# Optimization experiments

Hardware: AMD Instinct MI355X
Metric: run time of the kernel (lower is better)

The kernel has to match this reference:

```python
import jax, jax.numpy as jnp
import numpy as np

N = 50000       # num vertices
E_SEG = 80000   # num hyperedges
NNZ = 400000    # incidence pairs
FIN = 512       # input feature dim
H = 256         # MLP_hidden
C = 40          # num classes
NLAYER = 2      # All_num_layers
ALPHA = 0.5     # restart_alpha


def _w(k, shape):
    return jax.random.normal(k, shape, jnp.float32) * (1.0 / np.sqrt(shape[0]))


def setup_inputs() -> dict:
    key = jax.random.key(0)
    ks = jax.random.split(key, 12)
    return {
        "x": jax.random.normal(ks[0], (N, FIN), jnp.float32),
        "vertex": jax.random.randint(ks[1], (NNZ,), 0, N),
        "edges": jax.random.randint(ks[2], (NNZ,), 0, E_SEG),
        "lin_in_w": _w(ks[3], (FIN, H)), "lin_in_b": jnp.zeros((H,), jnp.float32),
        "w1": _w(ks[4], (H, H)),   "b1": jnp.zeros((H,), jnp.float32),
        "w2": _w(ks[5], (2 * H, H)), "b2": jnp.zeros((H,), jnp.float32),
        "w3": _w(ks[6], (H, H)),   "b3": jnp.zeros((H,), jnp.float32),
        "cls_w1": _w(ks[7], (H, H)), "cls_b1": jnp.zeros((H,), jnp.float32),
        "cls_w2": _w(ks[8], (H, C)), "cls_b2": jnp.zeros((C,), jnp.float32),
    }


def reference(x, vertex, edges, lin_in_w, lin_in_b, w1, b1, w2, b2, w3, b3,
              cls_w1, cls_b1, cls_w2, cls_b2):
    # input projection (dropout is identity at p=0)
    x = jax.nn.relu(x @ lin_in_w + lin_in_b)           # [N, H]
    x0 = x
    for _ in range(NLAYER):  # same conv weights reused each layer
        # W1 (1-layer MLP = Linear), gather to incidences
        xve = (x @ w1 + b1)[vertex]                    # [NNZ, H]
        # scatter-add to hyperedges
        xe = jax.ops.segment_sum(xve, edges, num_segments=E_SEG)  # [E, H]
        # gather back, concat with vertex feats, W2 (Linear on 2H)
        xev = jnp.concatenate([x[vertex], xe[edges]], axis=-1) @ w2 + b2  # [NNZ, H]
        # scatter-add to vertices
        xv = jax.ops.segment_sum(xev, vertex, num_segments=N)     # [N, H]
        # restart connection + W (Linear) + outer activation
        x = (1.0 - ALPHA) * xv + ALPHA * x0
        x = jax.nn.relu(x @ w3 + b3)
    # classifier MLP (2 layers: Linear -> relu -> Linear)
    h = jax.nn.relu(x @ cls_w1 + cls_b1)
    return h @ cls_w2 + cls_b2                          # [N, C]
```

## Files before the change

kernel.cpp:

```cpp
#include <hip/hip_runtime.h>
#include <hip/hip_bf16.h>
#include <cstdint>
#include <cstddef>

#define HD   256
#define NV   50000
#define NE   80000
#define NNZC 400000
#define FINC 512
#define NCLS 40

using bf16 = __hip_bfloat16;

typedef short bf16x8v __attribute__((ext_vector_type(8)));
typedef float f32x4   __attribute__((ext_vector_type(4)));

#define NCH_E ((NE + 1023) / 1024)
#define NCH_V ((NV + 1023) / 1024)

__device__ __forceinline__ float b2f(unsigned short u) {
    union { unsigned int i; float f; } c; c.i = ((unsigned int)u) << 16; return c.f;
}
__device__ __forceinline__ unsigned short f2b(float f) {
    union { float f; unsigned int i; } c; c.f = f;
    return (unsigned short)((c.i + 0x7FFFu + ((c.i >> 16) & 1u)) >> 16);
}
__device__ __forceinline__ float4 load4f(const bf16* p) {
    ushort4 u = *reinterpret_cast<const ushort4*>(p);
    return make_float4(b2f(u.x), b2f(u.y), b2f(u.z), b2f(u.w));
}
__device__ __forceinline__ void store4(bf16* p, float4 v) {
    ushort4 u; u.x = f2b(v.x); u.y = f2b(v.y); u.z = f2b(v.z); u.w = f2b(v.w);
    *reinterpret_cast<ushort4*>(p) = u;
}

__device__ __forceinline__ void gl_lds16(const bf16* g, short* l) {
    __builtin_amdgcn_global_load_lds(
        (const __attribute__((address_space(1))) unsigned int*)g,
        (__attribute__((address_space(3))) unsigned int*)l,
        16, 0, 0);
}

__global__ __launch_bounds__(256)
void fill0_k(unsigned int* __restrict__ p, long long n)
{
    long long i = (long long)blockIdx.x * 256 + threadIdx.x;
    long long stride = (long long)gridDim.x * 256;
    for (; i < n; i += stride) p[i] = 0u;
}

__global__ __launch_bounds__(256)
void hist_k(const int* __restrict__ vertex, const int* __restrict__ edges,
            int* __restrict__ cnt_v, int* __restrict__ cnt_e, int nnz)
{
    int i = blockIdx.x * 256 + threadIdx.x;
    if (i < nnz) {
        atomicAdd(&cnt_v[vertex[i]], 1);
        atomicAdd(&cnt_e[edges[i]], 1);
    }
}

__global__ __launch_bounds__(256)
void scan_part2_k(const int* __restrict__ cnt_e, int* __restrict__ off_e, int* __restrict__ part_e,
                  const int* __restrict__ cnt_v, int* __restrict__ off_v, int* __restrict__ part_v)
{
    const int* cnt; int* off; int* part; int n;
    if (blockIdx.y == 0) { cnt = cnt_e; off = off_e; part = part_e; n = NE; }
    else                 { cnt = cnt_v; off = off_v; part = part_v; n = NV; }
    int base = blockIdx.x * 1024;
    if (base >= n) return;
    __shared__ int s[256];
    int idx = base + threadIdx.x * 4;
    int v[4], sum = 0;
    #pragma unroll
    for (int j = 0; j < 4; ++j) { v[j] = (idx + j < n) ? cnt[idx + j] : 0; sum += v[j]; }
    s[threadIdx.x] = sum;
    __syncthreads();
    #pragma unroll
    for (int d = 1; d < 256; d <<= 1) {
        int t = (threadIdx.x >= d) ? s[threadIdx.x - d] : 0;
        __syncthreads();
        s[threadIdx.x] += t;
        __syncthreads();
    }
    int excl = s[threadIdx.x] - sum;
    #pragma unroll
    for (int j = 0; j < 4; ++j) {
        if (idx + j < n) off[idx + j] = excl;
        excl += v[j];
    }
    if (threadIdx.x == 255) part[blockIdx.x] = s[255];
}

__global__ __launch_bounds__(256)
void scan_top2_k(int* __restrict__ part_e, int* __restrict__ end_e,
                 int* __restrict__ part_v, int* __restrict__ end_v)
{
    int* part; int* endp; int nch;
    if (blockIdx.x == 0) { part = part_e; endp = end_e; nch = NCH_E; }
    else                 { part = part_v; endp = end_v; nch = NCH_V; }
    __shared__ int s[256];
    int v = (threadIdx.x < nch) ? part[threadIdx.x] : 0;
    s[threadIdx.x] = v;
    __syncthreads();
    #pragma unroll
    for (int d = 1; d < 256; d <<= 1) {
        int t = (threadIdx.x >= d) ? s[threadIdx.x - d] : 0;
        __syncthreads();
        s[threadIdx.x] += t;
        __syncthreads();
    }
    if (threadIdx.x < nch) part[threadIdx.x] = s[threadIdx.x] - v;
    if (threadIdx.x == 255) *endp = s[255];
}

__global__ __launch_bounds__(256)
void scan_addcur2_k(int* __restrict__ off_e, const int* __restrict__ part_e, int* __restrict__ cur_e,
                    int* __restrict__ off_v, const int* __restrict__ part_v, int* __restrict__ cur_v)
{
    int n; int* off; const int* part; int* cur;
    if (blockIdx.y == 0) { n = NE; off = off_e; part = part_e; cur = cur_e; }
    else                 { n = NV; off = off_v; part = part_v; cur = cur_v; }
    int i = blockIdx.x * 256 + threadIdx.x;
    if (i < n) { int o = off[i] + part[i >> 10]; off[i] = o; cur[i] = o; }
}

__global__ __launch_bounds__(256)
void csr_fill_k(const int* __restrict__ vertex, const int* __restrict__ edges,
                int* __restrict__ cur_e, int* __restrict__ cur_v,
                int* __restrict__ adj_e, int* __restrict__ adj_v, int nnz)
{
    int i = blockIdx.x * 256 + threadIdx.x;
    if (i >= nnz) return;
    int v = vertex[i], e = edges[i];
    adj_e[atomicAdd(&cur_e[e], 1)] = v;
    adj_v[atomicAdd(&cur_v[v], 1)] = e;
}

__global__ __launch_bounds__(256)
void dege2_k(const int* __restrict__ cnt_e, const int* __restrict__ adj_v,
             const int* __restrict__ off_v, int* __restrict__ dege2, int n)
{
    int v = blockIdx.x * 256 + threadIdx.x;
    if (v >= n) return;
    int s = 0;
    for (int j = off_v[v]; j < off_v[v + 1]; ++j) s += cnt_e[adj_v[j]];
    dege2[v] = s;
}

__global__ __launch_bounds__(256)
void b1w23_k(const float* __restrict__ b1, const unsigned short* __restrict__ W23bt,
             float* __restrict__ o)
{
    int n = threadIdx.x;
    float s = 0.f;
    for (int k = 0; k < 256; ++k) s += b1[k] * b2f(W23bt[n * 256 + k]);
    o[n] = s;
}

__global__ __launch_bounds__(256)
void prep_w_k(const float* __restrict__ lin_w, const float* __restrict__ w1,
              const float* __restrict__ w2, const float* __restrict__ w3,
              const float* __restrict__ cw1, const float* __restrict__ cw2,
              const float* __restrict__ b2,
              unsigned short* __restrict__ lin_wt, unsigned short* __restrict__ w1_nb,
              unsigned short* __restrict__ w2a_nb, unsigned short* __restrict__ w2b_nb,
              unsigned short* __restrict__ w3t, unsigned short* __restrict__ cw1t,
              unsigned short* __restrict__ cw2t, float* __restrict__ b2w3)
{
    int idx = blockIdx.x * 256 + threadIdx.x;
    if (idx < 131072) { int n = idx >> 9, k = idx & 511; lin_wt[idx] = f2b(lin_w[k * 256 + n]); return; }
    idx -= 131072;
    if (idx < 65536) { w1_nb[idx] = f2b(w1[idx]); return; }
    idx -= 65536;
    if (idx < 65536) { w2a_nb[idx] = f2b(w2[idx]); return; }
    idx -= 65536;
    if (idx < 65536) { w2b_nb[idx] = f2b(w2[65536 + idx]); return; }
    idx -= 65536;
    if (idx < 65536) { int n = idx >> 8, k = idx & 255; w3t[idx] = f2b(w3[k * 256 + n]); return; }
    idx -= 65536;
    if (idx < 65536) { int n = idx >> 8, k = idx & 255; cw1t[idx] = f2b(cw1[k * 256 + n]); return; }
    idx -= 65536;
    if (idx < 12288) { int n = idx >> 8, k = idx & 255; cw2t[idx] = f2b((n < NCLS) ? cw2[k * NCLS + n] : 0.f); return; }
    idx -= 12288;
    if (idx < 256) {
        float s = 0.f;
        for (int k = 0; k < 256; ++k) s += b2[k] * w3[k * 256 + idx];
        b2w3[idx] = s;
    }
}

template<int EPI, bool AF32>
__global__ __launch_bounds__(256)
void mgemm_k(const void* __restrict__ Agv, const bf16* __restrict__ Bt,
             const float* __restrict__ bias, const float* __restrict__ bias2,
             const int* __restrict__ deg, const int* __restrict__ dege2,
             const bf16* __restrict__ Sb, const bf16* __restrict__ z0b,
             const float* __restrict__ b2w3v, const float* __restrict__ b1w23v,
             bf16* __restrict__ Cg, bf16* __restrict__ Cg2, bf16* __restrict__ Cg3,
             int M, int K, int Nc)
{
    const int nbn = Nc >> 7;
    const int nbm = (M + 127) >> 7;
    const int p   = blockIdx.x;
    const int xcd = p & 7;
    const int q   = p >> 3;
    const int cblk = q % nbn;
    const int rblk = q / nbn;
    const int rb   = rblk * 8 + xcd;
    if (rb >= nbm) return;
    const int bn = cblk * 128;
    const int bm = rb * 128;

    __shared__ __align__(16) short As[128 * 64];
    __shared__ __align__(16) short Bs[128 * 64];

    const int t  = threadIdx.x;
    const int wv = t >> 6, l = t & 63;
    const int wr = wv >> 1, wc = wv & 1;
    const int l15 = l & 15;

    f32x4 acc[4][4];
    #pragma unroll
    for (int m = 0; m < 4; ++m)
        #pragma unroll
        for (int n = 0; n < 4; ++n)
            acc[m][n] = (f32x4){0.f, 0.f, 0.f, 0.f};

    const int brow8   = l >> 3;
    const int bcol_sw = (((l & 7) ^ (l >> 3)) * 8);

    for (int k0 = 0; k0 < K; k0 += 64) {
        if constexpr (AF32) {
            const float* Af = (const float*)Agv;
            #pragma unroll
            for (int pi = 0; pi < 4; ++pi) {
                int idx8 = pi * 256 + t;
                int row  = idx8 >> 3;
                int cg   = (idx8 & 7) * 8;
                int ga = bm + row; if (ga >= M) ga = M - 1;
                const float* src = Af + (size_t)ga * K + k0 + cg;
                f32x4 u = *reinterpret_cast<const f32x4*>(src);
                f32x4 v = *reinterpret_cast<const f32x4*>(src + 4);
                bf16x8v o;
                o[0] = (short)f2b(u[0]); o[1] = (short)f2b(u[1]);
                o[2] = (short)f2b(u[2]); o[3] = (short)f2b(u[3]);
                o[4] = (short)f2b(v[0]); o[5] = (short)f2b(v[1]);
                o[6] = (short)f2b(v[2]); o[7] = (short)f2b(v[3]);
                *reinterpret_cast<bf16x8v*>(As + row * 64 + (cg ^ ((row & 7) * 8))) = o;
            }
        } else {
            const bf16* Ab = (const bf16*)Agv;
            #pragma unroll
            for (int i = 0; i < 4; ++i) {
                int c = wv * 4 + i;
                int row = c * 8 + brow8;
                int ga = bm + row; if (ga >= M) ga = M - 1;
                gl_lds16(Ab + (size_t)ga * K + k0 + bcol_sw, As + c * 512);
            }
        }
        #pragma unroll
        for (int i = 0; i < 4; ++i) {
            int c = wv * 4 + i;
            int row = c * 8 + brow8;
            gl_lds16(Bt + (size_t)(bn + row) * K + k0 + bcol_sw, Bs + c * 512);
        }
        __syncthreads();

        #pragma unroll
        for (int ks = 0; ks < 2; ++ks) {
            bf16x8v a[4], b[4];
            const int kb = ks * 64 + (l >> 4) * 16;
            #pragma unroll
            for (int m = 0; m < 4; ++m) {
                int r = wr * 64 + m * 16 + l15;
                a[m] = *reinterpret_cast<const bf16x8v*>(
                           (const char*)As + r * 128 + (kb ^ ((r & 7) << 4)));
            }
            #pragma unroll
            for (int n = 0; n < 4; ++n) {
                int r = wc * 64 + n * 16 + l15;
                b[n] = *reinterpret_cast<const bf16x8v*>(
                           (const char*)Bs + r * 128 + (kb ^ ((r & 7) << 4)));
            }
            #pragma unroll
            for (int m = 0; m < 4; ++m)
                #pragma unroll
                for (int n = 0; n < 4; ++n)
                    acc[m][n] = __builtin_amdgcn_mfma_f32_16x16x32_bf16(a[m], b[n], acc[m][n], 0, 0, 0);
        }
        __syncthreads();
    }

    if (EPI == 3) {
        int oi = bn >> 8;
        bf16* CC = (oi == 0) ? Cg : (oi == 1) ? Cg2 : Cg3;
        const float* bb = (oi == 0) ? bias : (oi == 1) ? bias2 : nullptr;
        int cb = bn & 255;
        float bv[4];
        #pragma unroll
        for (int n = 0; n < 4; ++n)
            bv[n] = bb ? bb[cb + wc * 64 + n * 16 + l15] : 0.f;
        #pragma unroll
        for (int m = 0; m < 4; ++m) {
            #pragma unroll
            for (int i = 0; i < 4; ++i) {
                int row = bm + wr * 64 + m * 16 + (l >> 4) * 4 + i;
                if (row >= M) continue;
                size_t base = (size_t)row * 256 + cb + wc * 64 + l15;
                #pragma unroll
                for (int n = 0; n < 4; ++n)
                    reinterpret_cast<unsigned short*>(CC)[base + n * 16] = f2b(acc[m][n][i] + bv[n]);
            }
        }
    } else if (EPI == 4) {
        float bv[4], bw[4], bb1[4];
        #pragma unroll
        for (int n = 0; n < 4; ++n) {
            int col = bn + wc * 64 + n * 16 + l15;
            bv[n]  = bias[col];
            bw[n]  = b2w3v[col];
            bb1[n] = b1w23v[col];
        }
        #pragma unroll
        for (int m = 0; m < 4; ++m) {
            #pragma unroll
            for (int i = 0; i < 4; ++i) {
                int row = bm + wr * 64 + m * 16 + (l >> 4) * 4 + i;
                if (row >= M) continue;
                float d   = (float)deg[row];
                float de2 = (float)dege2[row];
                size_t base = (size_t)row * Nc + bn + wc * 64 + l15;
                #pragma unroll
                for (int n = 0; n < 4; ++n) {
                    size_t idx = base + (size_t)n * 16;
                    float sv = b2f(reinterpret_cast<const unsigned short*>(Sb)[idx]);
                    float zv = b2f(reinterpret_cast<const unsigned short*>(z0b)[idx]);
                    float v = 0.5f * (d * (sv + bw[n]) + acc[m][n][i] + de2 * bb1[n])
                              + 0.5f * zv + bv[n];
                    v = fmaxf(v, 0.f);
                    reinterpret_cast<unsigned short*>(Cg)[idx] = f2b(v);
                }
            }
        }
    } else {
        float bv[4];
        #pragma unroll
        for (int n = 0; n < 4; ++n)
            bv[n] = bias ? bias[bn + wc * 64 + n * 16 + l15] : 0.f;
        #pragma unroll
        for (int m = 0; m < 4; ++m) {
            #pragma unroll
            for (int i = 0; i < 4; ++i) {
                int row = bm + wr * 64 + m * 16 + (l >> 4) * 4 + i;
                if (row >= M) continue;
                size_t base = (size_t)row * Nc + bn + wc * 64 + l15;
                #pragma unroll
                for (int n = 0; n < 4; ++n) {
                    float v = acc[m][n][i] + bv[n];
                    if (EPI == 1) v = fmaxf(v, 0.f);
                    reinterpret_cast<unsigned short*>(Cg)[base + n * 16] = f2b(v);
                }
            }
        }
    }
}

__global__ __launch_bounds__(256)
void gather_sum_k(const bf16* __restrict__ src, const int* __restrict__ adj,
                  const int* __restrict__ off, bf16* __restrict__ dst, int nseg)
{
    int seg = blockIdx.x * 4 + (threadIdx.x >> 6);
    if (seg >= nseg) return;
    int lane = threadIdx.x & 63;
    int s0 = off[seg], s1 = off[seg + 1];
    float4 acc = make_float4(0.f, 0.f, 0.f, 0.f);
    int j = s0;
    for (; j + 4 <= s1; j += 4) {
        int r0 = adj[j], r1 = adj[j + 1], r2 = adj[j + 2], r3 = adj[j + 3];
        float4 v0 = load4f(src + (size_t)r0 * HD + lane * 4);
        float4 v1 = load4f(src + (size_t)r1 * HD + lane * 4);
        float4 v2 = load4f(src + (size_t)r2 * HD + lane * 4);
        float4 v3 = load4f(src + (size_t)r3 * HD + lane * 4);
        acc.x += (v0.x + v1.x) + (v2.x + v3.x);
        acc.y += (v0.y + v1.y) + (v2.y + v3.y);
        acc.z += (v0.z + v1.z) + (v2.z + v3.z);
        acc.w += (v0.w + v1.w) + (v2.w + v3.w);
    }
    for (; j < s1; ++j) {
        float4 v = load4f(src + (size_t)adj[j] * HD + lane * 4);
        acc.x += v.x; acc.y += v.y; acc.z += v.z; acc.w += v.w;
    }
    store4(dst + (size_t)seg * HD + lane * 4, acc);
}

__global__ __launch_bounds__(256)
void cls_mfma_k(const bf16* __restrict__ Hm, const bf16* __restrict__ Wt,
                const float* __restrict__ bias, float* __restrict__ out, int M)
{
    const int wv = threadIdx.x >> 6, l = threadIdx.x & 63;
    const int l15 = l & 15;
    const int r0 = blockIdx.x * 64 + wv * 16;
    f32x4 acc[3];
    #pragma unroll
    for (int n = 0; n < 3; ++n) acc[n] = (f32x4){0.f, 0.f, 0.f, 0.f};

    int arow = r0 + l15; if (arow >= M) arow = M - 1;
    const int ko = (l >> 4) * 8;
    for (int kk = 0; kk < HD; kk += 32) {
        bf16x8v a = *reinterpret_cast<const bf16x8v*>(Hm + (size_t)arow * HD + kk + ko);
        #pragma unroll
        for (int n = 0; n < 3; ++n) {
            bf16x8v b = *reinterpret_cast<const bf16x8v*>(Wt + (size_t)(n * 16 + l15) * HD + kk + ko);
            acc[n] = __builtin_amdgcn_mfma_f32_16x16x32_bf16(a, b, acc[n], 0, 0, 0);
        }
    }
    #pragma unroll
    for (int n = 0; n < 3; ++n) {
        int col = n * 16 + l15;
        if (col >= NCLS) continue;
        float bv = bias[col];
        #pragma unroll
        for (int i = 0; i < 4; ++i) {
            int row = r0 + (l >> 4) * 4 + i;
            if (row < M) out[(size_t)row * NCLS + col] = acc[n][i] + bv;
        }
    }
}

static inline int xcd_grid(int M, int Nc)
{
    int nbm = (M + 127) >> 7;
    int nbn = Nc >> 7;
    return nbn * (((nbm + 7) / 8) * 8);
}

extern "C" void kernel_launch(void* const* d_in, const int* in_sizes, int n_in,
                              void* d_out, int out_size, void* d_ws, size_t ws_size,
                              hipStream_t stream)
{
    const float* x_in   = (const float*)d_in[0];
    const int*   vertex = (const int*)d_in[1];
    const int*   edges  = (const int*)d_in[2];
    const float* lin_w  = (const float*)d_in[3];
    const float* lin_b  = (const float*)d_in[4];
    const float* w1     = (const float*)d_in[5];
    const float* b1     = (const float*)d_in[6];
    const float* w2     = (const float*)d_in[7];
    const float* b2     = (const float*)d_in[8];
    const float* w3     = (const float*)d_in[9];
    const float* b3     = (const float*)d_in[10];
    const float* cw1    = (const float*)d_in[11];
    const float* cb1    = (const float*)d_in[12];
    const float* cw2    = (const float*)d_in[13];
    const float* cb2    = (const float*)d_in[14];
    float* out = (float*)d_out;
    (void)in_sizes; (void)n_in; (void)out_size; (void)ws_size;

    char* ws = (char*)d_ws;
    const size_t nvhd = (size_t)NV * HD, nehd = (size_t)NE * HD;
    size_t off = 0;
    auto alloc = [&](size_t bytes) { char* p = ws + off; off += (bytes + 255) & ~(size_t)255; return p; };
    bf16* x0 = (bf16*)alloc(nvhd * 2);
    bf16* xA = (bf16*)alloc(nvhd * 2);
    bf16* E1 = (bf16*)alloc(nehd * 2);
    bf16* E2 = (bf16*)alloc(nehd * 2);
    bf16* S  = (bf16*)alloc(nvhd * 2);
    bf16* z0 = (bf16*)alloc(nvhd * 2);
    unsigned short* W23at  = (unsigned short*)alloc(2 * 256 * 256 * 2);
    unsigned short* w3t    = W23at + 65536;
    unsigned short* W23bt  = (unsigned short*)alloc(256 * 256 * 2);
    unsigned short* W123bt = (unsigned short*)alloc(256 * 256 * 2);
    unsigned short* w2ab   = (unsigned short*)alloc(512 * 256 * 2);
    unsigned short* w2a_nb = w2ab;
    unsigned short* w2b_nb = w2ab + 256 * 256;
    unsigned short* w1_nb  = (unsigned short*)alloc(256 * 256 * 2);
    unsigned short* lin_wt = (unsigned short*)alloc(256 * 512 * 2);
    unsigned short* cw1t   = (unsigned short*)alloc(256 * 256 * 2);
    unsigned short* cw2t   = (unsigned short*)alloc(48 * 256 * 2);
    float* b2w3  = (float*)alloc(256 * 4);
    float* b1w23 = (float*)alloc(256 * 4);
    int* cnt_e = (int*)alloc(NE * 4);
    int* cnt_v = (int*)alloc(NV * 4);
    int* dege2 = (int*)alloc(NV * 4);
    int* off_e = (int*)alloc((NE + 1) * 4);
    int* off_v = (int*)alloc((NV + 1) * 4);
    int* cur_e = (int*)alloc(NE * 4);
    int* cur_v = (int*)alloc(NV * 4);
    int* part_e = (int*)alloc(256 * 4);
    int* part_v = (int*)alloc(256 * 4);
    int* adj_e = (int*)alloc((size_t)NNZC * 4);
    int* adj_v = (int*)alloc((size_t)NNZC * 4);

    dim3 blk(256);

    fill0_k<<<128, blk, 0, stream>>>((unsigned int*)cnt_e, NE + NV);
    hist_k<<<(NNZC + 255) / 256, blk, 0, stream>>>(vertex, edges, cnt_v, cnt_e, NNZC);
    scan_part2_k<<<dim3(NCH_E, 2), blk, 0, stream>>>(cnt_e, off_e, part_e, cnt_v, off_v, part_v);
    scan_top2_k<<<2, blk, 0, stream>>>(part_e, off_e + NE, part_v, off_v + NV);
    scan_addcur2_k<<<dim3((NE + 255) / 256, 2), blk, 0, stream>>>(off_e, part_e, cur_e,
                                                                  off_v, part_v, cur_v);
    csr_fill_k<<<(NNZC + 255) / 256, blk, 0, stream>>>(vertex, edges, cur_e, cur_v, adj_e, adj_v, NNZC);
    dege2_k<<<(NV + 255) / 256, blk, 0, stream>>>(cnt_e, adj_v, off_v, dege2, NV);

    prep_w_k<<<1841, blk, 0, stream>>>(lin_w, w1, w2, w3, cw1, cw2, b2,
                                       lin_wt, w1_nb, w2a_nb, w2b_nb, w3t, cw1t, cw2t, b2w3);
    mgemm_k<3, false><<<xcd_grid(256, 512), blk, 0, stream>>>((const bf16*)w3t, (const bf16*)w2ab,
        nullptr, nullptr, nullptr, nullptr, nullptr, nullptr, nullptr, nullptr,
        (bf16*)W23at, (bf16*)W23bt, nullptr, 256, 256, 512);
    mgemm_k<0, false><<<xcd_grid(256, 256), blk, 0, stream>>>((const bf16*)W23bt, (const bf16*)w1_nb,
        nullptr, nullptr, nullptr, nullptr, nullptr, nullptr, nullptr, nullptr,
        (bf16*)W123bt, nullptr, nullptr, 256, 256, 256);
    b1w23_k<<<1, blk, 0, stream>>>(b1, W23bt, b1w23);

    mgemm_k<1, true><<<xcd_grid(NV, 256), blk, 0, stream>>>(x_in, (const bf16*)lin_wt,
        lin_b, nullptr, nullptr, nullptr, nullptr, nullptr, nullptr, nullptr,
        x0, nullptr, nullptr, NV, FINC, HD);

    const bf16* cur = x0;
    for (int layer = 0; layer < 2; ++layer) {
        if (layer == 0) {
            mgemm_k<3, false><<<xcd_grid(NV, 512), blk, 0, stream>>>(cur, (const bf16*)W23at,
                nullptr, nullptr, nullptr, nullptr, nullptr, nullptr, nullptr, nullptr,
                S, z0, nullptr, NV, HD, 512);
        } else {
            mgemm_k<0, false><<<xcd_grid(NV, 256), blk, 0, stream>>>(cur, (const bf16*)W23at,
                nullptr, nullptr, nullptr, nullptr, nullptr, nullptr, nullptr, nullptr,
                S, nullptr, nullptr, NV, HD, HD);
        }
        gather_sum_k<<<(NE + 3) / 4, blk, 0, stream>>>(cur, adj_e, off_e, E2, NE);
        gather_sum_k<<<(NV + 3) / 4, blk, 0, stream>>>(E2, adj_v, off_v, E1, NV);
        mgemm_k<4, false><<<xcd_grid(NV, 256), blk, 0, stream>>>(E1, (const bf16*)W123bt,
            b3, nullptr, cnt_v, dege2, S, z0, b2w3, b1w23,
            xA, nullptr, nullptr, NV, HD, HD);
        cur = xA;
    }

    mgemm_k<1, false><<<xcd_grid(NV, 256), blk, 0, stream>>>(xA, (const bf16*)cw1t,
        cb1, nullptr, nullptr, nullptr, nullptr, nullptr, nullptr, nullptr,
        E1, nullptr, nullptr, NV, HD, HD);
    cls_mfma_k<<<(NV + 63) / 64, blk, 0, stream>>>(E1, (const bf16*)cw2t, cb2, out, NV);
}
```

Measured before the change: 474.5 us.

## Store S and z0 intermediates in fragment-permuted layout for vectorized epilogue access

```diff
diff --git a/kernel.cpp b/kernel.cpp
--- a/kernel.cpp
+++ b/kernel.cpp
@@ -14,9 +14,11 @@
 
 typedef short bf16x8v __attribute__((ext_vector_type(8)));
 typedef float f32x4   __attribute__((ext_vector_type(4)));
+typedef unsigned short u16x8 __attribute__((ext_vector_type(8)));
 
 #define NCH_E ((NE + 1023) / 1024)
 #define NCH_V ((NV + 1023) / 1024)
+#define NBM_V ((NV + 127) / 128)
 
 __device__ __forceinline__ float b2f(unsigned short u) {
     union { unsigned int i; float f; } c; c.i = ((unsigned int)u) << 16; return c.f;
@@ -292,26 +294,23 @@
         __syncthreads();
     }
 
-    if (EPI == 3) {
+    if (EPI == 5) {
         int oi = bn >> 8;
-        bf16* CC = (oi == 0) ? Cg : (oi == 1) ? Cg2 : Cg3;
-        const float* bb = (oi == 0) ? bias : (oi == 1) ? bias2 : nullptr;
-        int cb = bn & 255;
-        float bv[4];
-        #pragma unroll
-        for (int n = 0; n < 4; ++n)
-            bv[n] = bb ? bb[cb + wc * 64 + n * 16 + l15] : 0.f;
+        bf16* CC = (oi == 0) ? Cg : Cg2;
+        int c2 = (bn >> 7) & 1;
+        unsigned short* P = (unsigned short*)CC + ((size_t)(rb * 2 + c2) * 256 + t) * 64;
         #pragma unroll
         for (int m = 0; m < 4; ++m) {
-            #pragma unroll
-            for (int i = 0; i < 4; ++i) {
-                int row = bm + wr * 64 + m * 16 + (l >> 4) * 4 + i;
-                if (row >= M) continue;
-                size_t base = (size_t)row * 256 + cb + wc * 64 + l15;
+            u16x8 o0, o1;
+            #pragma unroll
+            for (int n = 0; n < 2; ++n)
                 #pragma unroll
-                for (int n = 0; n < 4; ++n)
-                    reinterpret_cast<unsigned short*>(CC)[base + n * 16] = f2b(acc[m][n][i] + bv[n]);
-            }
+                for (int i = 0; i < 4; ++i) {
+                    o0[n * 4 + i] = f2b(acc[m][n][i]);
+                    o1[n * 4 + i] = f2b(acc[m][n + 2][i]);
+                }
+            *reinterpret_cast<u16x8*>(P + m * 16)     = o0;
+            *reinterpret_cast<u16x8*>(P + m * 16 + 8) = o1;
         }
     } else if (EPI == 4) {
         float bv[4], bw[4], bb1[4];
@@ -321,6 +320,14 @@
             bv[n]  = bias[col];
             bw[n]  = b2w3v[col];
             bb1[n] = b1w23v[col];
+        }
+        const unsigned short* Sp = (const unsigned short*)Sb + ((size_t)(rb * 2 + cblk) * 256 + t) * 64;
+        const unsigned short* Zp = (const unsigned short*)z0b + ((size_t)(rb * 2 + cblk) * 256 + t) * 64;
+        u16x8 sv8[8], zv8[8];
+        #pragma unroll
+        for (int j = 0; j < 8; ++j) {
+            sv8[j] = *reinterpret_cast<const u16x8*>(Sp + j * 8);
+            zv8[j] = *reinterpret_cast<const u16x8*>(Zp + j * 8);
         }
         #pragma unroll
         for (int m = 0; m < 4; ++m) {
@@ -333,14 +340,35 @@
                 size_t base = (size_t)row * Nc + bn + wc * 64 + l15;
                 #pragma unroll
                 for (int n = 0; n < 4; ++n) {
-                    size_t idx = base + (size_t)n * 16;
-                    float sv = b2f(reinterpret_cast<const unsigned short*>(Sb)[idx]);
-                    float zv = b2f(reinterpret_cast<const unsigned short*>(z0b)[idx]);
+                    int e = m * 16 + n * 4 + i;
+                    float sv = b2f(sv8[e >> 3][e & 7]);
+                    float zv = b2f(zv8[e >> 3][e & 7]);
                     float v = 0.5f * (d * (sv + bw[n]) + acc[m][n][i] + de2 * bb1[n])
                               + 0.5f * zv + bv[n];
                     v = fmaxf(v, 0.f);
-                    reinterpret_cast<unsigned short*>(Cg)[idx] = f2b(v);
+                    reinterpret_cast<unsigned short*>(Cg)[base + (size_t)n * 16] = f2b(v);
                 }
+            }
+        }
+    } else if (EPI == 3) {
+        int oi = bn >> 8;
+        bf16* CC = (oi == 0) ? Cg : (oi == 1) ? Cg2 : Cg3;
+        const float* bb = (oi == 0) ? bias : (oi == 1) ? bias2 : nullptr;
+        int cb = bn & 255;
+        float bv[4];
+        #pragma unroll
+        for (int n = 0; n < 4; ++n)
+            bv[n] = bb ? bb[cb + wc * 64 + n * 16 + l15] : 0.f;
+        #pragma unroll
+        for (int m = 0; m < 4; ++m) {
+            #pragma unroll
+            for (int i = 0; i < 4; ++i) {
+                int row = bm + wr * 64 + m * 16 + (l >> 4) * 4 + i;
+                if (row >= M) continue;
+                size_t base = (size_t)row * 256 + cb + wc * 64 + l15;
+                #pragma unroll
+                for (int n = 0; n < 4; ++n)
+                    reinterpret_cast<unsigned short*>(CC)[base + n * 16] = f2b(acc[m][n][i] + bv[n]);
             }
         }
     } else {
@@ -459,14 +487,15 @@
 
     char* ws = (char*)d_ws;
     const size_t nvhd = (size_t)NV * HD, nehd = (size_t)NE * HD;
+    const size_t permsz = (size_t)(NBM_V + 1) * 2 * 256 * 64;
     size_t off = 0;
     auto alloc = [&](size_t bytes) { char* p = ws + off; off += (bytes + 255) & ~(size_t)255; return p; };
     bf16* x0 = (bf16*)alloc(nvhd * 2);
     bf16* xA = (bf16*)alloc(nvhd * 2);
     bf16* E1 = (bf16*)alloc(nehd * 2);
     bf16* E2 = (bf16*)alloc(nehd * 2);
-    bf16* S  = (bf16*)alloc(nvhd * 2);
-    bf16* z0 = (bf16*)alloc(nvhd * 2);
+    bf16* S  = (bf16*)alloc(permsz * 2);
+    bf16* z0 = (bf16*)alloc(permsz * 2);
     unsigned short* W23at  = (unsigned short*)alloc(2 * 256 * 256 * 2);
     unsigned short* w3t    = W23at + 65536;
     unsigned short* W23bt  = (unsigned short*)alloc(256 * 256 * 2);
@@ -520,11 +549,11 @@
     const bf16* cur = x0;
     for (int layer = 0; layer < 2; ++layer) {
         if (layer == 0) {
-            mgemm_k<3, false><<<xcd_grid(NV, 512), blk, 0, stream>>>(cur, (const bf16*)W23at,
+            mgemm_k<5, false><<<xcd_grid(NV, 512), blk, 0, stream>>>(cur, (const bf16*)W23at,
                 nullptr, nullptr, nullptr, nullptr, nullptr, nullptr, nullptr, nullptr,
                 S, z0, nullptr, NV, HD, 512);
         } else {
-            mgemm_k<0, false><<<xcd_grid(NV, 256), blk, 0, stream>>>(cur, (const bf16*)W23at,
+            mgemm_k<5, false><<<xcd_grid(NV, 256), blk, 0, stream>>>(cur, (const bf16*)W23at,
                 nullptr, nullptr, nullptr, nullptr, nullptr, nullptr, nullptr, nullptr,
                 S, nullptr, nullptr, NV, HD, HD);
         }
```

Result: slower. 487.0 us (+2.6%).
